# Optimization experiments

Measured on AMD Instinct MI355X. Metric: run time of the kernel, lower is better.

The kernel has to match this reference:

```python
import jax, jax.numpy as jnp
import numpy as np

N_NODES = 100000
D = 50            # node embedding dim; concat -> in_dim = 2*D = 100
N_EDGES = 2000000
HIDDEN = 32


def setup_inputs() -> dict:
    key = jax.random.key(0)
    k_z, k_e, k_w1, k_w2 = jax.random.split(key, 4)
    z = jax.random.normal(k_z, (N_NODES, D), dtype=jnp.float32)
    edge_label_index = jax.random.randint(k_e, (2, N_EDGES), 0, N_NODES, dtype=jnp.int64)
    # Linear params (stored as [in, out] for x @ W + b)
    W1 = jax.random.normal(k_w1, (2 * D, HIDDEN), dtype=jnp.float32) * (1.0 / np.sqrt(2 * D))
    b1 = jnp.zeros((HIDDEN,), dtype=jnp.float32)
    W2 = jax.random.normal(k_w2, (HIDDEN, 1), dtype=jnp.float32) * (1.0 / np.sqrt(HIDDEN))
    b2 = jnp.zeros((1,), dtype=jnp.float32)
    return {"z": z, "edge_label_index": edge_label_index,
            "W1": W1, "b1": b1, "W2": W2, "b2": b2}


def reference(z, edge_label_index, W1, b1, W2, b2):
    # Gather src/dst node embeddings: [E, D] each
    src = z[edge_label_index[0]]
    dst = z[edge_label_index[1]]
    x = jnp.concatenate([src, dst], axis=1)          # [E, 2D]
    h = jax.nn.relu(x @ W1 + b1)                      # [E, HIDDEN]; dropout is identity in eval
    out = h @ W2 + b2                                 # [E, 1]
    return out.reshape(-1)                            # [E]
```

## Files before the change

### kernel.cpp

```cpp
#include <hip/hip_runtime.h>
#include <hip/hip_fp16.h>

#define D 50
#define HIDDEN 32
#define NB 32
#define ZROW 52

__global__ __launch_bounds__(256, 4) void node_proj_kernel(
        const float* __restrict__ z,
        const float* __restrict__ W1,
        const float* __restrict__ b1,
        __half2* __restrict__ P2,
        int n_nodes) {
    __shared__ float zs[NB * ZROW];

    const int tid  = threadIdx.x;
    const int base = blockIdx.x * NB;
    int nloc = n_nodes - base;
    if (nloc > NB) nloc = NB;

    const float2* src2 = (const float2*)(z + (size_t)base * D);
    const int nf2 = nloc * (D / 2);
    for (int i = tid; i < nf2; i += 256) {
        int row  = i / 25;
        int col2 = i - row * 25;
        *(float2*)(zs + row * ZROW + col2 * 2) = src2[i];
    }
    __syncthreads();

    const int lane = tid & 63;
    const int wv   = tid >> 6;
    const int j    = lane & 31;
    const int half = lane >> 5;

    float Breg[D];
    const float* wcol = W1 + (size_t)(half * D) * HIDDEN + j;
#pragma unroll
    for (int k = 0; k < D; ++k) Breg[k] = wcol[(size_t)k * HIDDEN];

    const float bias = half ? 0.0f : b1[j];

    int nlo = wv * (NB / 4);
    int nhi = nlo + (NB / 4);
    if (nhi > nloc) nhi = nloc;

    for (int nl = nlo; nl < nhi; ++nl) {
        const float4* zr4 = (const float4*)(zs + nl * ZROW);
        float acc = bias;
#pragma unroll
        for (int q = 0; q < 12; ++q) {
            float4 v = zr4[q];
            acc = fmaf(v.x, Breg[4 * q],     acc);
            acc = fmaf(v.y, Breg[4 * q + 1], acc);
            acc = fmaf(v.z, Breg[4 * q + 2], acc);
            acc = fmaf(v.w, Breg[4 * q + 3], acc);
        }
        float2 t = *(const float2*)(zs + nl * ZROW + 48);
        acc = fmaf(t.x, Breg[48], acc);
        acc = fmaf(t.y, Breg[49], acc);

        float nb2 = __shfl_xor(acc, 1);
        if ((lane & 1) == 0) {
            P2[(size_t)(base + nl) * 32 + (lane >> 1)] = __floats2half2_rn(acc, nb2);
        }
    }
}

__global__ void edge_mlp_kernel(const int* __restrict__ eidx,
                                const __half* __restrict__ P,
                                const float* __restrict__ W2,
                                const float* __restrict__ b2,
                                float* __restrict__ out,
                                int n_edges) {
    int t = blockIdx.x * blockDim.x + threadIdx.x;
    int e = t >> 2;
    int r = t & 3;
    if (e >= n_edges) return;

    int s = eidx[e];
    int d = eidx[n_edges + e];

    uint4 ua = *(const uint4*)(P + (size_t)s * 64 + r * 8);
    uint4 ub = *(const uint4*)(P + (size_t)d * 64 + 32 + r * 8);
    float4 w0 = *(const float4*)(W2 + r * 8);
    float4 w1 = *(const float4*)(W2 + r * 8 + 4);

    float2 a0 = __half22float2(*(const __half2*)&ua.x);
    float2 a1 = __half22float2(*(const __half2*)&ua.y);
    float2 a2 = __half22float2(*(const __half2*)&ua.z);
    float2 a3 = __half22float2(*(const __half2*)&ua.w);
    float2 b0 = __half22float2(*(const __half2*)&ub.x);
    float2 b1v = __half22float2(*(const __half2*)&ub.y);
    float2 b2v = __half22float2(*(const __half2*)&ub.z);
    float2 b3 = __half22float2(*(const __half2*)&ub.w);

    float acc = (r == 0) ? b2[0] : 0.0f;
    acc = fmaf(fmaxf(a0.x + b0.x,  0.0f), w0.x, acc);
    acc = fmaf(fmaxf(a0.y + b0.y,  0.0f), w0.y, acc);
    acc = fmaf(fmaxf(a1.x + b1v.x, 0.0f), w0.z, acc);
    acc = fmaf(fmaxf(a1.y + b1v.y, 0.0f), w0.w, acc);
    acc = fmaf(fmaxf(a2.x + b2v.x, 0.0f), w1.x, acc);
    acc = fmaf(fmaxf(a2.y + b2v.y, 0.0f), w1.y, acc);
    acc = fmaf(fmaxf(a3.x + b3.x,  0.0f), w1.z, acc);
    acc = fmaf(fmaxf(a3.y + b3.y,  0.0f), w1.w, acc);

    acc += __shfl_xor(acc, 1);
    acc += __shfl_xor(acc, 2);

    if (r == 0) out[e] = acc;
}

__global__ void edge_direct_kernel(const float* __restrict__ z,
                                   const int* __restrict__ eidx,
                                   const float* __restrict__ W1,
                                   const float* __restrict__ b1,
                                   const float* __restrict__ W2,
                                   const float* __restrict__ b2,
                                   float* __restrict__ out,
                                   int n_edges) {
    int e = blockIdx.x * blockDim.x + threadIdx.x;
    if (e >= n_edges) return;
    int s = eidx[e];
    int d = eidx[n_edges + e];
    const float* zs = z + (size_t)s * D;
    const float* zd = z + (size_t)d * D;
    float acc = b2[0];
    for (int j = 0; j < HIDDEN; ++j) {
        float h = b1[j];
        for (int k = 0; k < D; ++k) {
            h = fmaf(zs[k], W1[(size_t)k * HIDDEN + j], h);
            h = fmaf(zd[k], W1[(size_t)(D + k) * HIDDEN + j], h);
        }
        acc = fmaf(fmaxf(h, 0.0f), W2[j], acc);
    }
    out[e] = acc;
}

extern "C" void kernel_launch(void* const* d_in, const int* in_sizes, int n_in,
                              void* d_out, int out_size, void* d_ws, size_t ws_size,
                              hipStream_t stream) {
    const float* z    = (const float*)d_in[0];
    const int*   eidx = (const int*)d_in[1];
    const float* W1   = (const float*)d_in[2];
    const float* b1   = (const float*)d_in[3];
    const float* W2   = (const float*)d_in[4];
    const float* b2   = (const float*)d_in[5];
    float*       out  = (float*)d_out;

    const int n_nodes = in_sizes[0] / D;
    const int n_edges = in_sizes[1] / 2;

    const size_t p_bytes = (size_t)n_nodes * 64 * sizeof(__half);

    if (p_bytes <= ws_size) {
        __half* P = (__half*)d_ws;

        int blocks1 = (n_nodes + NB - 1) / NB;
        node_proj_kernel<<<blocks1, 256, 0, stream>>>(z, W1, b1, (__half2*)P,
                                                      n_nodes);

        long long total2 = (long long)n_edges * 4;
        int blocks2 = (int)((total2 + 255) / 256);
        edge_mlp_kernel<<<blocks2, 256, 0, stream>>>(eidx, P, W2, b2, out, n_edges);
    } else {
        int blocks = (n_edges + 255) / 256;
        edge_direct_kernel<<<blocks, 256, 0, stream>>>(z, eidx, W1, b1, W2, b2,
                                                       out, n_edges);
    }
}
```

Measured before the change: 76.50 us.

## Restructure node projection: node row in registers, broadcast transposed weights

Adds a small kernel that transposes W1 into a padded [64 x 64] layout with the bias folded in. The node projection kernel now gives each lane one node, holds that node's 50 features in registers, and loops over pairs of output columns. Weights are read through wave-uniform loads from the transposed buffer instead of per-lane strided register preloads. This is meant to remove the per-node serial loop and the shuffles of the old mapping, at the cost of an extra launch and strided per-node half2 stores.

Measured after the change: 126.4 us. 65.2% more time.

```diff
diff --git a/kernel.cpp b/kernel.cpp
--- a/kernel.cpp
+++ b/kernel.cpp
@@ -3,65 +3,84 @@
 
 #define D 50
 #define HIDDEN 32
-#define NB 32
-#define ZROW 52
+#define NPB 128
+#define ZPAD 52
+#define WROW 64
 
-__global__ __launch_bounds__(256, 4) void node_proj_kernel(
+__global__ void build_w1t_kernel(const float* __restrict__ W1,
+                                 const float* __restrict__ b1,
+                                 float* __restrict__ W1T) {
+    int i = blockIdx.x * blockDim.x + threadIdx.x;
+    if (i >= 64 * WROW) return;
+    int j = i >> 6;
+    int k = i & (WROW - 1);
+    float v = 0.0f;
+    if (k < D) {
+        v = (j < 32) ? W1[(size_t)k * HIDDEN + j]
+                     : W1[(size_t)(D + k) * HIDDEN + (j - 32)];
+    } else if (k == D) {
+        v = (j < 32) ? b1[j] : 0.0f;
+    }
+    W1T[i] = v;
+}
+
+__global__ __launch_bounds__(256, 2) void node_proj_kernel(
         const float* __restrict__ z,
-        const float* __restrict__ W1,
-        const float* __restrict__ b1,
+        const float* __restrict__ W1T,
         __half2* __restrict__ P2,
         int n_nodes) {
-    __shared__ float zs[NB * ZROW];
+    __shared__ __align__(16) float zs[NPB * ZPAD];
 
     const int tid  = threadIdx.x;
-    const int base = blockIdx.x * NB;
+    const int base = blockIdx.x * NPB;
     int nloc = n_nodes - base;
-    if (nloc > NB) nloc = NB;
+    if (nloc > NPB) nloc = NPB;
 
     const float2* src2 = (const float2*)(z + (size_t)base * D);
     const int nf2 = nloc * (D / 2);
     for (int i = tid; i < nf2; i += 256) {
-        int row  = i / 25;
-        int col2 = i - row * 25;
-        *(float2*)(zs + row * ZROW + col2 * 2) = src2[i];
+        int row = i / 25;
+        int c   = i - row * 25;
+        *(float2*)(zs + row * ZPAD + 2 * c) = src2[i];
     }
     __syncthreads();
 
-    const int lane = tid & 63;
-    const int wv   = tid >> 6;
-    const int j    = lane & 31;
-    const int half = lane >> 5;
+    const int lane  = tid & 63;
+    const int wv    = tid >> 6;
+    const int grp   = wv & 1;
+    const int jbase = (wv >> 1) * 16;
+    const int nl    = grp * 64 + lane;
+    const int node  = base + nl;
+    const bool act  = (node < n_nodes) && (nl < nloc);
 
-    float Breg[D];
-    const float* wcol = W1 + (size_t)(half * D) * HIDDEN + j;
+    float zr[D];
+    const float4* row4 = (const float4*)(zs + nl * ZPAD);
 #pragma unroll
-    for (int k = 0; k < D; ++k) Breg[k] = wcol[(size_t)k * HIDDEN];
+    for (int q = 0; q < 12; ++q) {
+        float4 v = row4[q];
+        zr[4 * q]     = v.x;
+        zr[4 * q + 1] = v.y;
+        zr[4 * q + 2] = v.z;
+        zr[4 * q + 3] = v.w;
+    }
+    {
+        float2 t = *(const float2*)(zs + nl * ZPAD + 48);
+        zr[48] = t.x;
+        zr[49] = t.y;
+    }
 
-    const float bias = half ? 0.0f : b1[j];
-
-    int nlo = wv * (NB / 4);
-    int nhi = nlo + (NB / 4);
-    if (nhi > nloc) nhi = nloc;
-
-    for (int nl = nlo; nl < nhi; ++nl) {
-        const float4* zr4 = (const float4*)(zs + nl * ZROW);
-        float acc = bias;
+    for (int jp = jbase; jp < jbase + 16; ++jp) {
+        const float* w0 = W1T + (size_t)(2 * jp) * WROW;
+        const float* w1 = W1T + (size_t)(2 * jp + 1) * WROW;
+        float a0 = w0[D];
+        float a1 = w1[D];
 #pragma unroll
-        for (int q = 0; q < 12; ++q) {
-            float4 v = zr4[q];
-            acc = fmaf(v.x, Breg[4 * q],     acc);
-            acc = fmaf(v.y, Breg[4 * q + 1], acc);
-            acc = fmaf(v.z, Breg[4 * q + 2], acc);
-            acc = fmaf(v.w, Breg[4 * q + 3], acc);
+        for (int k = 0; k < D; ++k) {
+            a0 = fmaf(zr[k], w0[k], a0);
+            a1 = fmaf(zr[k], w1[k], a1);
         }
-        float2 t = *(const float2*)(zs + nl * ZROW + 48);
-        acc = fmaf(t.x, Breg[48], acc);
-        acc = fmaf(t.y, Breg[49], acc);
-
-        float nb2 = __shfl_xor(acc, 1);
-        if ((lane & 1) == 0) {
-            P2[(size_t)(base + nl) * 32 + (lane >> 1)] = __floats2half2_rn(acc, nb2);
+        if (act) {
+            P2[(size_t)node * 32 + jp] = __floats2half2_rn(a0, a1);
         }
     }
 }
@@ -150,13 +169,17 @@
     const int n_nodes = in_sizes[0] / D;
     const int n_edges = in_sizes[1] / 2;
 
-    const size_t p_bytes = (size_t)n_nodes * 64 * sizeof(__half);
+    const size_t p_bytes   = (size_t)n_nodes * 64 * sizeof(__half);
+    const size_t w1t_bytes = (size_t)64 * WROW * sizeof(float);
 
-    if (p_bytes <= ws_size) {
-        __half* P = (__half*)d_ws;
+    if (p_bytes + w1t_bytes <= ws_size) {
+        __half* P   = (__half*)d_ws;
+        float*  W1T = (float*)((char*)d_ws + p_bytes);
 
-        int blocks1 = (n_nodes + NB - 1) / NB;
-        node_proj_kernel<<<blocks1, 256, 0, stream>>>(z, W1, b1, (__half2*)P,
+        build_w1t_kernel<<<(64 * WROW + 255) / 256, 256, 0, stream>>>(W1, b1, W1T);
+
+        int blocks1 = (n_nodes + NPB - 1) / NPB;
+        node_proj_kernel<<<blocks1, 256, 0, stream>>>(z, W1T, (__half2*)P,
                                                       n_nodes);
 
         long long total2 = (long long)n_edges * 4;
```
